# Kernel optimization log

Hardware: AMD Instinct MI355X
Metric: run time of the kernel (lower is better)

Reference implementation:

```python
import jax, jax.numpy as jnp
import numpy as np


def setup_inputs() -> dict:
    key = jax.random.key(0)
    ks = jax.random.split(key, 5)
    bt, c, h, w = 64, 64, 32, 32
    x = jax.random.normal(ks[0], (bt, c, h, w), dtype=jnp.float32)
    qkv_w = jax.random.normal(ks[1], (3 * c, c), dtype=jnp.float32) * 0.05
    qkv_b = jax.random.normal(ks[2], (3 * c,), dtype=jnp.float32) * 0.05
    tqk_w = jax.random.normal(ks[3], (2 * c, c, 3, 1, 1), dtype=jnp.float32) * 0.05
    tqk_b = jax.random.normal(ks[4], (2 * c,), dtype=jnp.float32) * 0.05
    return {"x": x, "qkv_w": qkv_w, "qkv_b": qkv_b,
            "tqk_w": tqk_w, "tqk_b": tqk_b, "n_segment": 8}


def reference(x, qkv_w, qkv_b, tqk_w, tqk_b, n_segment):
    bt, c, h, w = x.shape
    t = n_segment
    b = bt // t
    n = h * w
    scale = c ** (-0.5)

    # 1x1 conv -> qkv, then tokens: [bt, n, c]
    qkv = jnp.einsum('bchw,oc->bohw', x, qkv_w) + qkv_b[None, :, None, None]
    q, k, v = jnp.split(qkv, 3, axis=1)
    q, k, v = (a.transpose(0, 2, 3, 1).reshape(bt, n, c) for a in (q, k, v))

    # pixel (spatial) attention over n tokens
    pixel_dots = jnp.einsum('bic,bjc->bij', q, k) * scale          # [bt, n, n]
    pixel_attn = jax.nn.softmax(pixel_dots, axis=-1)
    pixel_out = jnp.einsum('bij,bjd->bid', pixel_attn, v)          # [bt, n, c]

    # channel attention over c channels
    chan_dots = jnp.einsum('bic,bik->bck', q, k) * scale           # [bt, c, c]
    chan_attn = jax.nn.softmax(chan_dots, axis=-1)
    chan_out = jnp.einsum('bij,bdj->bdi', chan_attn, v)            # [bt, n, c]

    x_hat = pixel_out + chan_out                                   # [bt, n, c]
    # '(b t) (h w) c -> b c t h w'
    x_hat = x_hat.reshape(b, t, h, w, c).transpose(0, 4, 1, 2, 3)

    # Conv3d kernel (3,1,1), padding (1,0,0): temporal-only conv
    t_qk = jax.lax.conv_general_dilated(
        x_hat, tqk_w, window_strides=(1, 1, 1),
        padding=[(1, 1), (0, 0), (0, 0)],
        dimension_numbers=('NCDHW', 'OIDHW', 'NCDHW'))
    t_qk = t_qk + tqk_b[None, :, None, None, None]                 # [b, 2c, t, h, w]
    tq, tk = jnp.split(t_qk, 2, axis=1)
    # 'b c t h w -> b t (c h w)'
    tq = tq.transpose(0, 2, 1, 3, 4).reshape(b, t, c * n)
    tk = tk.transpose(0, 2, 1, 3, 4).reshape(b, t, c * n)
    # tv: '(b t) (h w) c -> b t (c h w)'
    tv = v.reshape(b, t, h, w, c).transpose(0, 1, 4, 2, 3).reshape(b, t, c * n)

    dots = jnp.einsum('bid,bjd->bij', tq, tk)                      # [b, t, t] (no scale, as source)
    attn = jax.nn.softmax(dots, axis=-1)
    out = jnp.einsum('bkt,btd->bkd', attn, tv)                     # [b, t, c*n]
    out = out.reshape(b, t, c, h, w).reshape(bt, c, h, w)
    return out
```

## Files before the change

### kernel.cpp

```cpp
#include <hip/hip_runtime.h>

#define SCALE 0.125f

typedef _Float16 f16;
typedef _Float16 f16x8 __attribute__((ext_vector_type(8)));
typedef float f32x4 __attribute__((ext_vector_type(4)));

#define MFMA16(A,B,C) __builtin_amdgcn_mfma_f32_16x16x32_f16(A,B,C,0,0,0)

__device__ __forceinline__ float dp4(const float a[4], const float b[4], float acc) {
    acc = fmaf(a[0], b[0], acc);
    acc = fmaf(a[1], b[1], acc);
    acc = fmaf(a[2], b[2], acc);
    acc = fmaf(a[3], b[3], acc);
    return acc;
}

__device__ __forceinline__ int sw(int row) {
    return ((row & 7) ^ ((row >> 3) & 7)) << 4;
}

__global__ __launch_bounds__(256) void k_qkv(const float* __restrict__ x,
                                             const float* __restrict__ w,
                                             const float* __restrict__ bias,
                                             f16* __restrict__ q,
                                             f16* __restrict__ k,
                                             f16* __restrict__ v,
                                             f16* __restrict__ vt) {
    __shared__ float xs[64][64];
    __shared__ float ws[192][65];
    __shared__ f16 vts[4096];
    const int bt = blockIdx.y, pos0 = blockIdx.x * 64;
    const int tid = threadIdx.x;

    for (int it = 0; it < 16; ++it) {
        int idx = it * 256 + tid;
        int ci = idx >> 6, p = idx & 63;
        xs[ci][p] = x[(bt * 64 + ci) * 1024 + pos0 + p];
    }
    for (int it = 0; it < 48; ++it) {
        int idx = it * 256 + tid;
        ws[idx / 64][idx % 64] = w[idx];
    }
    __syncthreads();

    const int oc = tid & 63, grp = tid >> 6;
    float accq[16], acck[16], accv[16];
    const float bq = bias[oc], bk = bias[64 + oc], bv = bias[128 + oc];
#pragma unroll
    for (int p = 0; p < 16; ++p) { accq[p] = bq; acck[p] = bk; accv[p] = bv; }

    for (int ci = 0; ci < 64; ++ci) {
        float wq = ws[oc][ci], wk = ws[64 + oc][ci], wv = ws[128 + oc][ci];
        const float4* xr = (const float4*)&xs[ci][grp * 16];
#pragma unroll
        for (int p4 = 0; p4 < 4; ++p4) {
            float xa[4];
            *(float4*)xa = xr[p4];
#pragma unroll
            for (int e = 0; e < 4; ++e) {
                int p = p4 * 4 + e;
                accq[p] = fmaf(wq, xa[e], accq[p]);
                acck[p] = fmaf(wk, xa[e], acck[p]);
                accv[p] = fmaf(wv, xa[e], accv[p]);
            }
        }
    }
#pragma unroll
    for (int p = 0; p < 16; ++p) {
        int pos = pos0 + grp * 16 + p;
        int base = (bt * 1024 + pos) * 64 + oc;
        f16 vh = (f16)accv[p];
        q[base] = (f16)(accq[p] * SCALE);
        k[base] = (f16)acck[p];
        v[base] = vh;
        int col = grp * 16 + p;
        *(f16*)((char*)vts + oc * 128 + ((col * 2) ^ sw(oc))) = vh;
    }
    __syncthreads();
#pragma unroll
    for (int it = 0; it < 2; ++it) {
        int s = it * 256 + tid;
        int row = s >> 3, c8 = s & 7;
        f16x8 val = *(const f16x8*)((char*)vts + row * 128 + ((c8 * 16) ^ sw(row)));
        *(f16x8*)(vt + (bt * 64 + row) * 1024 + pos0 + c8 * 8) = val;
    }
}

__global__ __launch_bounds__(256) void k_chan_part(const f16* __restrict__ q,
                                                   const f16* __restrict__ k,
                                                   float* __restrict__ partials) {
    __shared__ float qs[64][68];
    __shared__ float ks[64][68];
    const int pc = blockIdx.x, bt = blockIdx.y, tid = threadIdx.x;
    const int ti = tid >> 4, tj = tid & 15;
    float acc[4][4] = {{0.f}};

    for (int ch = 0; ch < 4; ++ch) {
        int p0 = pc * 256 + ch * 64;
        __syncthreads();
        for (int it = 0; it < 2; ++it) {
            int e8 = it * 256 + tid;
            int p = e8 >> 3, c8 = e8 & 7;
            f16x8 qv = *(const f16x8*)(q + (bt * 1024 + p0 + p) * 64 + c8 * 8);
            f16x8 kv = *(const f16x8*)(k + (bt * 1024 + p0 + p) * 64 + c8 * 8);
            float4 qlo = make_float4((float)qv[0], (float)qv[1], (float)qv[2], (float)qv[3]);
            float4 qhi = make_float4((float)qv[4], (float)qv[5], (float)qv[6], (float)qv[7]);
            float4 klo = make_float4((float)kv[0], (float)kv[1], (float)kv[2], (float)kv[3]);
            float4 khi = make_float4((float)kv[4], (float)kv[5], (float)kv[6], (float)kv[7]);
            *(float4*)&qs[p][c8 * 8]     = qlo;
            *(float4*)&qs[p][c8 * 8 + 4] = qhi;
            *(float4*)&ks[p][c8 * 8]     = klo;
            *(float4*)&ks[p][c8 * 8 + 4] = khi;
        }
        __syncthreads();
#pragma unroll 8
        for (int p = 0; p < 64; ++p) {
            float qa[4], ka[4];
            *(float4*)qa = *(const float4*)&qs[p][ti * 4];
            *(float4*)ka = *(const float4*)&ks[p][tj * 4];
#pragma unroll
            for (int r = 0; r < 4; ++r)
#pragma unroll
                for (int c = 0; c < 4; ++c)
                    acc[r][c] = fmaf(qa[r], ka[c], acc[r][c]);
        }
    }
#pragma unroll
    for (int r = 0; r < 4; ++r) {
        float4 o4 = make_float4(acc[r][0], acc[r][1], acc[r][2], acc[r][3]);
        *(float4*)&partials[((bt * 4 + pc) * 64 + ti * 4 + r) * 64 + tj * 4] = o4;
    }
}

__global__ __launch_bounds__(256) void k_chan_red(const float* __restrict__ partials,
                                                  f16* __restrict__ cattn) {
    const int bt = blockIdx.x, tid = threadIdx.x;
    const int i = tid >> 2, q4 = tid & 3;
    float s[16];
#pragma unroll
    for (int jj = 0; jj < 16; ++jj) s[jj] = 0.f;
#pragma unroll
    for (int pc = 0; pc < 4; ++pc) {
        const float4* src = (const float4*)(partials + ((bt * 4 + pc) * 64 + i) * 64 + q4 * 16);
#pragma unroll
        for (int f4 = 0; f4 < 4; ++f4) {
            float a[4];
            *(float4*)a = src[f4];
#pragma unroll
            for (int e = 0; e < 4; ++e) s[f4 * 4 + e] += a[e];
        }
    }
    float m = -1e30f;
#pragma unroll
    for (int jj = 0; jj < 16; ++jj) m = fmaxf(m, s[jj]);
    m = fmaxf(m, __shfl_xor(m, 1, 64));
    m = fmaxf(m, __shfl_xor(m, 2, 64));
    float e[16], sum = 0.f;
#pragma unroll
    for (int jj = 0; jj < 16; ++jj) { e[jj] = __expf(s[jj] - m); sum += e[jj]; }
    sum += __shfl_xor(sum, 1, 64);
    sum += __shfl_xor(sum, 2, 64);
    float inv = 1.f / sum;
    f16x8 o0, o1;
#pragma unroll
    for (int jj = 0; jj < 8; ++jj) { o0[jj] = (f16)(e[jj] * inv); o1[jj] = (f16)(e[8 + jj] * inv); }
    f16* dst = cattn + (bt * 64 + i) * 64 + q4 * 16;
    *(f16x8*)dst = o0;
    *(f16x8*)(dst + 8) = o1;
}

__global__ __launch_bounds__(256) void k_pixel(const f16* __restrict__ q,
                                               const f16* __restrict__ k,
                                               const f16* __restrict__ v,
                                               const f16* __restrict__ vt,
                                               const f16* __restrict__ cattn,
                                               f16* __restrict__ xh,
                                               f16* __restrict__ xl) {
    __shared__ f16 kv_s[2][8192];
    __shared__ f16 p_s[8192];

    const int bt = blockIdx.x, row0 = blockIdx.y * 128;
    const int tid = threadIdx.x;
    const int wv = tid >> 6;
    const int ln = tid & 15;
    const int kgrp = (tid >> 4) & 3;
    const int r2 = tid >> 3, c8 = tid & 7;

    f16x8 k0, k1, v0, v1;
    const f16* kbase = k + bt * 1024 * 64;
    const f16* vtbase = vt + (size_t)bt * 65536;

    auto issue = [&](int ch) {
        const f16* kg = kbase + ch * 64 * 64;
        const f16* vtg = vtbase + ch * 64;
        k0 = *(const f16x8*)(kg + r2 * 64 + c8 * 8);
        k1 = *(const f16x8*)(kg + (r2 + 32) * 64 + c8 * 8);
        v0 = *(const f16x8*)(vtg + r2 * 1024 + c8 * 8);
        v1 = *(const f16x8*)(vtg + (r2 + 32) * 1024 + c8 * 8);
    };
    auto commit = [&](int buf) {
        char* kb = (char*)&kv_s[buf][0];
        char* vb = (char*)&kv_s[buf][4096];
        *(f16x8*)(kb + r2 * 128 + ((c8 * 16) ^ sw(r2))) = k0;
        *(f16x8*)(kb + (r2 + 32) * 128 + ((c8 * 16) ^ sw(r2 + 32))) = k1;
        *(f16x8*)(vb + r2 * 128 + ((c8 * 16) ^ sw(r2))) = v0;
        *(f16x8*)(vb + (r2 + 32) * 128 + ((c8 * 16) ^ sw(r2 + 32))) = v1;
    };

    issue(0);
    {
        const f16* qg = q + (bt * 1024 + row0) * 64;
#pragma unroll
        for (int p = 0; p < 4; ++p) {
            int e8 = p * 256 + tid;
            int rr = e8 >> 3, cc = e8 & 7;
            f16x8 val = *(const f16x8*)(qg + rr * 64 + cc * 8);
            *(f16x8*)((char*)p_s + rr * 128 + ((cc * 16) ^ sw(rr))) = val;
        }
    }
    __syncthreads();
    f16x8 qa[2][2];
#pragma unroll
    for (int rt = 0; rt < 2; ++rt) {
        int rr = rt * 64 + 16 * wv + ln;
#pragma unroll
        for (int kb = 0; kb < 2; ++kb)
            qa[rt][kb] = *(const f16x8*)((char*)p_s + rr * 128 + (((kb * 4 + kgrp) * 16) ^ sw(rr)));
    }
    commit(0);
    issue(1);
    __syncthreads();

    f32x4 out[2][4];
    float lr[2][4];
#pragma unroll
    for (int rt = 0; rt < 2; ++rt)
#pragma unroll
        for (int ct = 0; ct < 4; ++ct) {
            out[rt][ct] = (f32x4){0.f, 0.f, 0.f, 0.f};
            lr[rt][ct] = 0.f;
        }

    for (int ch = 0; ch < 16; ++ch) {
        const char* kb = (const char*)&kv_s[ch & 1][0];
        const char* vb = (const char*)&kv_s[ch & 1][4096];

        f16x8 kf[4][2];
#pragma unroll
        for (int jt = 0; jt < 4; ++jt)
#pragma unroll
            for (int kb2 = 0; kb2 < 2; ++kb2) {
                int jr = jt * 16 + ln;
                kf[jt][kb2] = *(const f16x8*)(kb + jr * 128 + (((kb2 * 4 + kgrp) * 16) ^ sw(jr)));
            }
#pragma unroll
        for (int rt = 0; rt < 2; ++rt) {
            f32x4 sx[4];
#pragma unroll
            for (int jt = 0; jt < 4; ++jt) sx[jt] = (f32x4){0.f, 0.f, 0.f, 0.f};
#pragma unroll
            for (int jt = 0; jt < 4; ++jt)
#pragma unroll
                for (int kb2 = 0; kb2 < 2; ++kb2)
                    sx[jt] = MFMA16(qa[rt][kb2], kf[jt][kb2], sx[jt]);
#pragma unroll
            for (int jt = 0; jt < 4; ++jt)
#pragma unroll
                for (int r = 0; r < 4; ++r) {
                    float p = __expf(sx[jt][r]);
                    lr[rt][r] += p;
                    int prow = rt * 64 + 16 * wv + kgrp * 4 + r;
                    int pcol = jt * 16 + ln;
                    *(f16*)((char*)p_s + prow * 128 + ((pcol * 2) ^ sw(prow))) = (f16)p;
                }
        }
        f16x8 vf[4][2];
#pragma unroll
        for (int ct = 0; ct < 4; ++ct)
#pragma unroll
            for (int kb2 = 0; kb2 < 2; ++kb2) {
                int cr = ct * 16 + ln;
                vf[ct][kb2] = *(const f16x8*)(vb + cr * 128 + (((kb2 * 4 + kgrp) * 16) ^ sw(cr)));
            }
#pragma unroll
        for (int rt = 0; rt < 2; ++rt) {
            int rr = rt * 64 + 16 * wv + ln;
            f16x8 pa[2];
#pragma unroll
            for (int kb2 = 0; kb2 < 2; ++kb2)
                pa[kb2] = *(const f16x8*)((char*)p_s + rr * 128 + (((kb2 * 4 + kgrp) * 16) ^ sw(rr)));
#pragma unroll
            for (int ct = 0; ct < 4; ++ct)
#pragma unroll
                for (int kb2 = 0; kb2 < 2; ++kb2)
                    out[rt][ct] = MFMA16(pa[kb2], vf[ct][kb2], out[rt][ct]);
        }
        if (ch < 15) {
            commit((ch + 1) & 1);
            if (ch < 14) issue(ch + 2);
        }
        __syncthreads();
    }

#pragma unroll
    for (int mask = 1; mask < 16; mask <<= 1)
#pragma unroll
        for (int rt = 0; rt < 2; ++rt)
#pragma unroll
            for (int r = 0; r < 4; ++r) lr[rt][r] += __shfl_xor(lr[rt][r], mask, 64);
#pragma unroll
    for (int rt = 0; rt < 2; ++rt)
#pragma unroll
        for (int r = 0; r < 4; ++r) {
            float inv = 1.f / lr[rt][r];
#pragma unroll
            for (int ct = 0; ct < 4; ++ct) out[rt][ct][r] *= inv;
        }

    {
        f16* cs = &kv_s[0][0];
        const f16* cg = cattn + bt * 4096;
#pragma unroll
        for (int p = 0; p < 2; ++p) {
            int e8 = p * 256 + tid;
            int rr = e8 >> 3, cc = e8 & 7;
            f16x8 cv = *(const f16x8*)(cg + rr * 64 + cc * 8);
            *(f16x8*)((char*)cs + rr * 128 + ((cc * 16) ^ sw(rr))) = cv;
        }
        const f16* vg = v + (bt * 1024 + row0) * 64;
#pragma unroll
        for (int p = 0; p < 4; ++p) {
            int e8 = p * 256 + tid;
            int rr = e8 >> 3, cc = e8 & 7;
            f16x8 vv = *(const f16x8*)(vg + rr * 64 + cc * 8);
            *(f16x8*)((char*)p_s + rr * 128 + ((cc * 16) ^ sw(rr))) = vv;
        }
    }
    __syncthreads();
    {
        const char* cs = (const char*)&kv_s[0][0];
        f16x8 cb[4][2];
#pragma unroll
        for (int it = 0; it < 4; ++it)
#pragma unroll
            for (int kb2 = 0; kb2 < 2; ++kb2) {
                int ir = it * 16 + ln;
                cb[it][kb2] = *(const f16x8*)(cs + ir * 128 + (((kb2 * 4 + kgrp) * 16) ^ sw(ir)));
            }
#pragma unroll
        for (int rt = 0; rt < 2; ++rt) {
            int rr = rt * 64 + 16 * wv + ln;
            f16x8 va[2];
#pragma unroll
            for (int kb2 = 0; kb2 < 2; ++kb2)
                va[kb2] = *(const f16x8*)((char*)p_s + rr * 128 + (((kb2 * 4 + kgrp) * 16) ^ sw(rr)));
#pragma unroll
            for (int it = 0; it < 4; ++it)
#pragma unroll
                for (int kb2 = 0; kb2 < 2; ++kb2)
                    out[rt][it] = MFMA16(va[kb2], cb[it][kb2], out[rt][it]);
        }
    }

#pragma unroll
    for (int rt = 0; rt < 2; ++rt)
#pragma unroll
        for (int ct = 0; ct < 4; ++ct)
#pragma unroll
            for (int r = 0; r < 4; ++r) {
                float val = out[rt][ct][r];
                f16 h = (f16)val;
                int idx = (bt * 1024 + row0 + rt * 64 + 16 * wv + kgrp * 4 + r) * 64 + ct * 16 + ln;
                xh[idx] = h;
                xl[idx] = (f16)(val - (float)h);
            }
}

__global__ void k_wprep(const float* __restrict__ w, f16* __restrict__ wsplit) {
    int d = blockIdx.x * 256 + threadIdx.x;
    int j = d & 7, oc = (d >> 3) & 127, kg = (d >> 10) & 3, kc = d >> 12;
    int K = kc * 32 + kg * 8 + j;
    int dt = K >> 6, ci = K & 63;
    float wf = w[(oc * 64 + ci) * 3 + dt];
    f16 h = (f16)wf;
    wsplit[d] = h;
    wsplit[24576 + d] = (f16)(wf - (float)h);
}

__global__ __launch_bounds__(256) void k_tconv(const f16* __restrict__ xh,
                                               const f16* __restrict__ xl,
                                               const f16* __restrict__ wsplit,
                                               const float* __restrict__ bias,
                                               float* __restrict__ tq,
                                               float* __restrict__ tk) {
    __shared__ f16 xs[2][3][4096];
    const int bt = blockIdx.y, pos0 = blockIdx.x * 64;
    const int b = bt >> 3, t = bt & 7;
    const int tid = threadIdx.x;
    const int wvid = tid >> 6, ln = tid & 15, kgrp = (tid >> 4) & 3;

    for (int dt = 0; dt < 3; ++dt) {
        int tt = t + dt - 1;
        bool ok = (tt >= 0) && (tt < 8);
        const f16* srch = xh + ((b * 8 + tt) * 1024 + pos0) * 64;
        const f16* srcl = xl + ((b * 8 + tt) * 1024 + pos0) * 64;
#pragma unroll
        for (int p = 0; p < 2; ++p) {
            int e8 = p * 256 + tid;
            int r2 = e8 >> 3, c8 = e8 & 7;
            f16x8 vh = {0, 0, 0, 0, 0, 0, 0, 0};
            f16x8 vl = {0, 0, 0, 0, 0, 0, 0, 0};
            if (ok) {
                vh = *(const f16x8*)(srch + r2 * 64 + c8 * 8);
                vl = *(const f16x8*)(srcl + r2 * 64 + c8 * 8);
            }
            int byte = r2 * 128 + ((c8 * 16) ^ sw(r2));
            *(f16x8*)((char*)&xs[0][dt][0] + byte) = vh;
            *(f16x8*)((char*)&xs[1][dt][0] + byte) = vl;
        }
    }

    f16x8 bh[2][6], bl[2][6];
#pragma unroll
    for (int og = 0; og < 2; ++og) {
        int oc = wvid * 32 + og * 16 + ln;
#pragma unroll
        for (int kc = 0; kc < 6; ++kc) {
            int idx = (kc * 4 + kgrp) * 1024 + oc * 8;
            bh[og][kc] = *(const f16x8*)(wsplit + idx);
            bl[og][kc] = *(const f16x8*)(wsplit + 24576 + idx);
        }
    }
    __syncthreads();

#pragma unroll
    for (int pg = 0; pg < 4; ++pg) {
        f16x8 ah[6], al[6];
        int rr = pg * 16 + ln;
#pragma unroll
        for (int kc = 0; kc < 6; ++kc) {
            int dt = kc >> 1;
            int ci0 = (kc & 1) * 32 + kgrp * 8;
            int byte = rr * 128 + ((ci0 * 2) ^ sw(rr));
            ah[kc] = *(const f16x8*)((char*)&xs[0][dt][0] + byte);
            al[kc] = *(const f16x8*)((char*)&xs[1][dt][0] + byte);
        }
#pragma unroll
        for (int og = 0; og < 2; ++og) {
            int oc = wvid * 32 + og * 16 + ln;
            float bv = bias[oc];
            f32x4 acc = {bv, bv, bv, bv};
#pragma unroll
            for (int kc = 0; kc < 6; ++kc) {
                acc = MFMA16(ah[kc], bh[og][kc], acc);
                acc = MFMA16(al[kc], bh[og][kc], acc);
                acc = MFMA16(ah[kc], bl[og][kc], acc);
            }
            float* dst = (oc < 64) ? tq : tk;
            int orow = oc & 63;
            int pos = pos0 + pg * 16 + kgrp * 4;
            *(float4*)&dst[(bt * 64 + orow) * 1024 + pos] =
                make_float4(acc[0], acc[1], acc[2], acc[3]);
        }
    }
}

__global__ __launch_bounds__(256) void k_tdots(const float* __restrict__ tq,
                                               const float* __restrict__ tk,
                                               float* __restrict__ partials) {
    __shared__ float qs[8][516];
    __shared__ float ks[8][516];
    const int ch = blockIdx.x, b = blockIdx.y;
    const int tid = threadIdx.x;
    const int d0 = ch * 512;

    for (int it = 0; it < 4; ++it) {
        int f4 = it * 256 + tid;
        int i = f4 >> 7, d4 = f4 & 127;
        *(float4*)&qs[i][d4 * 4] = *(const float4*)(tq + (size_t)(b * 8 + i) * 65536 + d0 + d4 * 4);
        *(float4*)&ks[i][d4 * 4] = *(const float4*)(tk + (size_t)(b * 8 + i) * 65536 + d0 + d4 * 4);
    }
    __syncthreads();

    const int p = tid >> 2, sub = tid & 3;
    const int i = p >> 3, j = p & 7;
    float acc = 0.f;
#pragma unroll 8
    for (int d4 = 0; d4 < 32; ++d4) {
        int off = (d4 * 4 + sub) * 4;
        float qa[4], ka[4];
        *(float4*)qa = *(const float4*)&qs[i][off];
        *(float4*)ka = *(const float4*)&ks[j][off];
        acc = dp4(qa, ka, acc);
    }
    acc += __shfl_xor(acc, 1, 64);
    acc += __shfl_xor(acc, 2, 64);
    if (sub == 0) partials[(b * 128 + ch) * 64 + p] = acc;
}

__global__ void k_tsm(const float* __restrict__ partials, float* __restrict__ ta) {
    const int b = blockIdx.x, tid = threadIdx.x;
    float s = 0.f;
    for (int ch = 0; ch < 128; ++ch) s += partials[(b * 128 + ch) * 64 + tid];
    float m = s;
#pragma unroll
    for (int mask = 1; mask < 8; mask <<= 1) m = fmaxf(m, __shfl_xor(m, mask, 64));
    float e = __expf(s - m);
    float sum = e;
#pragma unroll
    for (int mask = 1; mask < 8; mask <<= 1) sum += __shfl_xor(sum, mask, 64);
    ta[b * 64 + tid] = e / sum;
}

__global__ __launch_bounds__(256) void k_tout(const f16* __restrict__ v,
                                              const float* __restrict__ ta,
                                              float* __restrict__ outp) {
    __shared__ float ot[64][65];
    const int pt = blockIdx.x, kk = blockIdx.y, b = blockIdx.z;
    const int pos0 = pt * 64;
    const int tid = threadIdx.x;
    const int cc = tid & 63, grp = tid >> 6;
    float a[8];
#pragma unroll
    for (int t = 0; t < 8; ++t) a[t] = ta[(b * 8 + kk) * 8 + t];
    float acc[16] = {0.f};
#pragma unroll
    for (int t = 0; t < 8; ++t) {
        const f16* vb = v + ((size_t)(b * 8 + t) * 1024 + pos0) * 64 + cc;
#pragma unroll
        for (int pp = 0; pp < 16; ++pp)
            acc[pp] = fmaf(a[t], (float)vb[(grp * 16 + pp) * 64], acc[pp]);
    }
#pragma unroll
    for (int pp = 0; pp < 16; ++pp) ot[cc][grp * 16 + pp] = acc[pp];
    __syncthreads();
    for (int it = 0; it < 16; ++it) {
        int idx = it * 256 + tid;
        int c2 = idx >> 6, p2 = idx & 63;
        outp[((b * 8 + kk) * 64 + c2) * 1024 + pos0 + p2] = ot[c2][p2];
    }
}

extern "C" void kernel_launch(void* const* d_in, const int* in_sizes, int n_in,
                              void* d_out, int out_size, void* d_ws, size_t ws_size,
                              hipStream_t stream) {
    const float* x     = (const float*)d_in[0];
    const float* qkv_w = (const float*)d_in[1];
    const float* qkv_b = (const float*)d_in[2];
    const float* tqk_w = (const float*)d_in[3];
    const float* tqk_b = (const float*)d_in[4];
    float* outp = (float*)d_out;

    char* wsb = (char*)d_ws;
    f16*   q        = (f16*)wsb;
    f16*   k        = (f16*)(wsb + (8u << 20));
    f16*   v        = (f16*)(wsb + (16u << 20));
    f16*   cattn    = (f16*)(wsb + (24u << 20));
    float* tpart    = (float*)(wsb + (24u << 20) + (1u << 19));
    float* ta       = (float*)(wsb + (24u << 20) + (1u << 19) + (1u << 18));
    f16*   wsplit   = (f16*)(wsb + (24u << 20) + (1u << 19) + (1u << 18) + 8192);
    f16*   xhat_hi  = (f16*)(wsb + (25u << 20));
    f16*   xhat_lo  = (f16*)(wsb + (33u << 20));
    float* cpart    = (float*)(wsb + (41u << 20));
    float* tq       = (float*)wsb;
    float* tk       = (float*)(wsb + (41u << 20));
    f16*   vt       = (f16*)(wsb + (57u << 20));

    k_qkv      <<<dim3(16, 64), 256, 0, stream>>>(x, qkv_w, qkv_b, q, k, v, vt);
    k_wprep    <<<dim3(96), 256, 0, stream>>>(tqk_w, wsplit);
    k_chan_part<<<dim3(4, 64), 256, 0, stream>>>(q, k, cpart);
    k_chan_red <<<dim3(64), 256, 0, stream>>>(cpart, cattn);
    k_pixel    <<<dim3(64, 8), 256, 0, stream>>>(q, k, v, vt, cattn, xhat_hi, xhat_lo);
    k_tconv    <<<dim3(16, 64), 256, 0, stream>>>(xhat_hi, xhat_lo, wsplit, tqk_b, tq, tk);
    k_tdots    <<<dim3(128, 8), 256, 0, stream>>>(tq, tk, tpart);
    k_tsm      <<<dim3(8), 64, 0, stream>>>(tpart, ta);
    k_tout     <<<dim3(16, 8, 8), 256, 0, stream>>>(v, ta, outp);
}
```

Before: 183.7 us.

## Fuse weight prep into qkv, softmax into tout, transpose pixel S layout

Folds the temporal-conv weight split into extra blocks of the qkv kernel and folds the temporal softmax reduction into the output kernel, removing two launches. The output kernel now handles four query frames per block, reusing each V load across them. The pixel attention kernel computes S transposed (K as the A operand), so each lane holds contiguous P columns. It writes them as packed f16x2 into a padded 144-byte-stride buffer and reduces row sums with fewer shuffles. The cost is redundant partial-sum reduction per tout block and more registers in tout.

```diff
diff --git a/kernel.cpp b/kernel.cpp
--- a/kernel.cpp
+++ b/kernel.cpp
@@ -3,6 +3,7 @@
 #define SCALE 0.125f
 
 typedef _Float16 f16;
+typedef _Float16 f16x2 __attribute__((ext_vector_type(2)));
 typedef _Float16 f16x8 __attribute__((ext_vector_type(8)));
 typedef float f32x4 __attribute__((ext_vector_type(4)));
 
@@ -23,15 +24,31 @@
 __global__ __launch_bounds__(256) void k_qkv(const float* __restrict__ x,
                                              const float* __restrict__ w,
                                              const float* __restrict__ bias,
+                                             const float* __restrict__ tqkw,
                                              f16* __restrict__ q,
                                              f16* __restrict__ k,
                                              f16* __restrict__ v,
-                                             f16* __restrict__ vt) {
+                                             f16* __restrict__ vt,
+                                             f16* __restrict__ wsplit) {
+    const int tid = threadIdx.x;
+    if (blockIdx.y == 64) {
+#pragma unroll
+        for (int it = 0; it < 6; ++it) {
+            int d = blockIdx.x * 1536 + it * 256 + tid;
+            int j = d & 7, oc = (d >> 3) & 127, kg = (d >> 10) & 3, kc = d >> 12;
+            int K = kc * 32 + kg * 8 + j;
+            int dt = K >> 6, ci = K & 63;
+            float wf = tqkw[(oc * 64 + ci) * 3 + dt];
+            f16 h = (f16)wf;
+            wsplit[d] = h;
+            wsplit[24576 + d] = (f16)(wf - (float)h);
+        }
+        return;
+    }
     __shared__ float xs[64][64];
     __shared__ float ws[192][65];
     __shared__ f16 vts[4096];
     const int bt = blockIdx.y, pos0 = blockIdx.x * 64;
-    const int tid = threadIdx.x;
 
     for (int it = 0; it < 16; ++it) {
         int idx = it * 256 + tid;
@@ -178,7 +195,7 @@
                                                f16* __restrict__ xh,
                                                f16* __restrict__ xl) {
     __shared__ f16 kv_s[2][8192];
-    __shared__ f16 p_s[8192];
+    __shared__ char p_raw[18432];
 
     const int bt = blockIdx.x, row0 = blockIdx.y * 128;
     const int tid = threadIdx.x;
@@ -216,7 +233,7 @@
             int e8 = p * 256 + tid;
             int rr = e8 >> 3, cc = e8 & 7;
             f16x8 val = *(const f16x8*)(qg + rr * 64 + cc * 8);
-            *(f16x8*)((char*)p_s + rr * 128 + ((cc * 16) ^ sw(rr))) = val;
+            *(f16x8*)(p_raw + rr * 128 + ((cc * 16) ^ sw(rr))) = val;
         }
     }
     __syncthreads();
@@ -226,21 +243,18 @@
         int rr = rt * 64 + 16 * wv + ln;
 #pragma unroll
         for (int kb = 0; kb < 2; ++kb)
-            qa[rt][kb] = *(const f16x8*)((char*)p_s + rr * 128 + (((kb * 4 + kgrp) * 16) ^ sw(rr)));
+            qa[rt][kb] = *(const f16x8*)(p_raw + rr * 128 + (((kb * 4 + kgrp) * 16) ^ sw(rr)));
     }
     commit(0);
     issue(1);
     __syncthreads();
 
     f32x4 out[2][4];
-    float lr[2][4];
+    float lr[2] = {0.f, 0.f};
 #pragma unroll
     for (int rt = 0; rt < 2; ++rt)
 #pragma unroll
-        for (int ct = 0; ct < 4; ++ct) {
-            out[rt][ct] = (f32x4){0.f, 0.f, 0.f, 0.f};
-            lr[rt][ct] = 0.f;
-        }
+        for (int ct = 0; ct < 4; ++ct) out[rt][ct] = (f32x4){0.f, 0.f, 0.f, 0.f};
 
     for (int ch = 0; ch < 16; ++ch) {
         const char* kb = (const char*)&kv_s[ch & 1][0];
@@ -256,6 +270,8 @@
             }
 #pragma unroll
         for (int rt = 0; rt < 2; ++rt) {
+            int prow = rt * 64 + wv * 16 + ln;
+            char* pb = p_raw + prow * 144;
             f32x4 sx[4];
 #pragma unroll
             for (int jt = 0; jt < 4; ++jt) sx[jt] = (f32x4){0.f, 0.f, 0.f, 0.f};
@@ -263,17 +279,18 @@
             for (int jt = 0; jt < 4; ++jt)
 #pragma unroll
                 for (int kb2 = 0; kb2 < 2; ++kb2)
-                    sx[jt] = MFMA16(qa[rt][kb2], kf[jt][kb2], sx[jt]);
-#pragma unroll
-            for (int jt = 0; jt < 4; ++jt)
-#pragma unroll
-                for (int r = 0; r < 4; ++r) {
-                    float p = __expf(sx[jt][r]);
-                    lr[rt][r] += p;
-                    int prow = rt * 64 + 16 * wv + kgrp * 4 + r;
-                    int pcol = jt * 16 + ln;
-                    *(f16*)((char*)p_s + prow * 128 + ((pcol * 2) ^ sw(prow))) = (f16)p;
-                }
+                    sx[jt] = MFMA16(kf[jt][kb2], qa[rt][kb2], sx[jt]);
+#pragma unroll
+            for (int jt = 0; jt < 4; ++jt) {
+                float p0 = __expf(sx[jt][0]), p1 = __expf(sx[jt][1]);
+                float p2 = __expf(sx[jt][2]), p3 = __expf(sx[jt][3]);
+                lr[rt] += (p0 + p1) + (p2 + p3);
+                f16x2 w0, w1;
+                w0[0] = (f16)p0; w0[1] = (f16)p1;
+                w1[0] = (f16)p2; w1[1] = (f16)p3;
+                *(f16x2*)(pb + (jt * 8 + kgrp * 2) * 4) = w0;
+                *(f16x2*)(pb + (jt * 8 + kgrp * 2 + 1) * 4) = w1;
+            }
         }
         f16x8 vf[4][2];
 #pragma unroll
@@ -285,11 +302,11 @@
             }
 #pragma unroll
         for (int rt = 0; rt < 2; ++rt) {
-            int rr = rt * 64 + 16 * wv + ln;
+            int prow = rt * 64 + wv * 16 + ln;
             f16x8 pa[2];
 #pragma unroll
             for (int kb2 = 0; kb2 < 2; ++kb2)
-                pa[kb2] = *(const f16x8*)((char*)p_s + rr * 128 + (((kb2 * 4 + kgrp) * 16) ^ sw(rr)));
+                pa[kb2] = *(const f16x8*)(p_raw + prow * 144 + (kb2 * 16 + kgrp * 4) * 4);
 #pragma unroll
             for (int ct = 0; ct < 4; ++ct)
 #pragma unroll
@@ -303,20 +320,21 @@
         __syncthreads();
     }
 
-#pragma unroll
-    for (int mask = 1; mask < 16; mask <<= 1)
-#pragma unroll
-        for (int rt = 0; rt < 2; ++rt)
-#pragma unroll
-            for (int r = 0; r < 4; ++r) lr[rt][r] += __shfl_xor(lr[rt][r], mask, 64);
-#pragma unroll
-    for (int rt = 0; rt < 2; ++rt)
-#pragma unroll
-        for (int r = 0; r < 4; ++r) {
-            float inv = 1.f / lr[rt][r];
-#pragma unroll
-            for (int ct = 0; ct < 4; ++ct) out[rt][ct][r] *= inv;
-        }
+    float invr[2][4];
+#pragma unroll
+    for (int rt = 0; rt < 2; ++rt) {
+        float l = lr[rt];
+        l += __shfl_xor(l, 16, 64);
+        l += __shfl_xor(l, 32, 64);
+        float inv = 1.f / l;
+#pragma unroll
+        for (int r = 0; r < 4; ++r)
+            invr[rt][r] = __shfl(inv, kgrp * 4 + r, 64);
+#pragma unroll
+        for (int r = 0; r < 4; ++r)
+#pragma unroll
+            for (int ct = 0; ct < 4; ++ct) out[rt][ct][r] *= invr[rt][r];
+    }
 
     {
         f16* cs = &kv_s[0][0];
@@ -334,7 +352,7 @@
             int e8 = p * 256 + tid;
             int rr = e8 >> 3, cc = e8 & 7;
             f16x8 vv = *(const f16x8*)(vg + rr * 64 + cc * 8);
-            *(f16x8*)((char*)p_s + rr * 128 + ((cc * 16) ^ sw(rr))) = vv;
+            *(f16x8*)(p_raw + rr * 128 + ((cc * 16) ^ sw(rr))) = vv;
         }
     }
     __syncthreads();
@@ -354,7 +372,7 @@
             f16x8 va[2];
 #pragma unroll
             for (int kb2 = 0; kb2 < 2; ++kb2)
-                va[kb2] = *(const f16x8*)((char*)p_s + rr * 128 + (((kb2 * 4 + kgrp) * 16) ^ sw(rr)));
+                va[kb2] = *(const f16x8*)(p_raw + rr * 128 + (((kb2 * 4 + kgrp) * 16) ^ sw(rr)));
 #pragma unroll
             for (int it = 0; it < 4; ++it)
 #pragma unroll
@@ -375,17 +393,6 @@
                 xh[idx] = h;
                 xl[idx] = (f16)(val - (float)h);
             }
-}
-
-__global__ void k_wprep(const float* __restrict__ w, f16* __restrict__ wsplit) {
-    int d = blockIdx.x * 256 + threadIdx.x;
-    int j = d & 7, oc = (d >> 3) & 127, kg = (d >> 10) & 3, kc = d >> 12;
-    int K = kc * 32 + kg * 8 + j;
-    int dt = K >> 6, ci = K & 63;
-    float wf = w[(oc * 64 + ci) * 3 + dt];
-    f16 h = (f16)wf;
-    wsplit[d] = h;
-    wsplit[24576 + d] = (f16)(wf - (float)h);
 }
 
 __global__ __launch_bounds__(256) void k_tconv(const f16* __restrict__ xh,
@@ -499,46 +506,77 @@
     if (sub == 0) partials[(b * 128 + ch) * 64 + p] = acc;
 }
 
-__global__ void k_tsm(const float* __restrict__ partials, float* __restrict__ ta) {
-    const int b = blockIdx.x, tid = threadIdx.x;
-    float s = 0.f;
-    for (int ch = 0; ch < 128; ++ch) s += partials[(b * 128 + ch) * 64 + tid];
-    float m = s;
-#pragma unroll
-    for (int mask = 1; mask < 8; mask <<= 1) m = fmaxf(m, __shfl_xor(m, mask, 64));
-    float e = __expf(s - m);
-    float sum = e;
-#pragma unroll
-    for (int mask = 1; mask < 8; mask <<= 1) sum += __shfl_xor(sum, mask, 64);
-    ta[b * 64 + tid] = e / sum;
-}
-
 __global__ __launch_bounds__(256) void k_tout(const f16* __restrict__ v,
-                                              const float* __restrict__ ta,
+                                              const float* __restrict__ partials,
                                               float* __restrict__ outp) {
+    __shared__ float sred[32][9];
+    __shared__ float ta_s[4][8];
     __shared__ float ot[64][65];
-    const int pt = blockIdx.x, kk = blockIdx.y, b = blockIdx.z;
+    const int pt = blockIdx.x, kq = blockIdx.y, b = blockIdx.z;
     const int pos0 = pt * 64;
     const int tid = threadIdx.x;
+
+    {
+        const int pair = tid & 31, grp8 = tid >> 5;
+        const int i = kq * 4 + (pair >> 3), j = pair & 7;
+        float s = 0.f;
+#pragma unroll
+        for (int c = 0; c < 16; ++c)
+            s += partials[(b * 128 + grp8 * 16 + c) * 64 + i * 8 + j];
+        sred[pair][grp8] = s;
+    }
+    __syncthreads();
+    if (tid < 32) {
+        float t = 0.f;
+#pragma unroll
+        for (int g = 0; g < 8; ++g) t += sred[tid][g];
+        float m = t;
+        m = fmaxf(m, __shfl_xor(m, 1, 64));
+        m = fmaxf(m, __shfl_xor(m, 2, 64));
+        m = fmaxf(m, __shfl_xor(m, 4, 64));
+        float e = __expf(t - m);
+        float se = e;
+        se += __shfl_xor(se, 1, 64);
+        se += __shfl_xor(se, 2, 64);
+        se += __shfl_xor(se, 4, 64);
+        ta_s[tid >> 3][tid & 7] = e / se;
+    }
+    __syncthreads();
+
     const int cc = tid & 63, grp = tid >> 6;
-    float a[8];
-#pragma unroll
-    for (int t = 0; t < 8; ++t) a[t] = ta[(b * 8 + kk) * 8 + t];
-    float acc[16] = {0.f};
+    float tar[4][8];
+#pragma unroll
+    for (int kk = 0; kk < 4; ++kk)
+#pragma unroll
+        for (int t = 0; t < 8; ++t) tar[kk][t] = ta_s[kk][t];
+    float acc[4][16];
+#pragma unroll
+    for (int kk = 0; kk < 4; ++kk)
+#pragma unroll
+        for (int pp = 0; pp < 16; ++pp) acc[kk][pp] = 0.f;
 #pragma unroll
     for (int t = 0; t < 8; ++t) {
         const f16* vb = v + ((size_t)(b * 8 + t) * 1024 + pos0) * 64 + cc;
 #pragma unroll
-        for (int pp = 0; pp < 16; ++pp)
-            acc[pp] = fmaf(a[t], (float)vb[(grp * 16 + pp) * 64], acc[pp]);
-    }
-#pragma unroll
-    for (int pp = 0; pp < 16; ++pp) ot[cc][grp * 16 + pp] = acc[pp];
-    __syncthreads();
-    for (int it = 0; it < 16; ++it) {
-        int idx = it * 256 + tid;
-        int c2 = idx >> 6, p2 = idx & 63;
-        outp[((b * 8 + kk) * 64 + c2) * 1024 + pos0 + p2] = ot[c2][p2];
+        for (int pp = 0; pp < 16; ++pp) {
+            float vv = (float)vb[(grp * 16 + pp) * 64];
+#pragma unroll
+            for (int kk = 0; kk < 4; ++kk)
+                acc[kk][pp] = fmaf(tar[kk][t], vv, acc[kk][pp]);
+        }
+    }
+#pragma unroll
+    for (int kk = 0; kk < 4; ++kk) {
+        __syncthreads();
+#pragma unroll
+        for (int pp = 0; pp < 16; ++pp) ot[cc][grp * 16 + pp] = acc[kk][pp];
+        __syncthreads();
+        float* dst = outp + ((size_t)(b * 8 + kq * 4 + kk) * 64) * 1024 + pos0;
+        for (int it = 0; it < 16; ++it) {
+            int idx = it * 256 + tid;
+            int c2 = idx >> 6, p2 = idx & 63;
+            dst[c2 * 1024 + p2] = ot[c2][p2];
+        }
     }
 }
 
@@ -558,7 +596,6 @@
     f16*   v        = (f16*)(wsb + (16u << 20));
     f16*   cattn    = (f16*)(wsb + (24u << 20));
     float* tpart    = (float*)(wsb + (24u << 20) + (1u << 19));
-    float* ta       = (float*)(wsb + (24u << 20) + (1u << 19) + (1u << 18));
     f16*   wsplit   = (f16*)(wsb + (24u << 20) + (1u << 19) + (1u << 18) + 8192);
     f16*   xhat_hi  = (f16*)(wsb + (25u << 20));
     f16*   xhat_lo  = (f16*)(wsb + (33u << 20));
@@ -567,13 +604,11 @@
     float* tk       = (float*)(wsb + (41u << 20));
     f16*   vt       = (f16*)(wsb + (57u << 20));
 
-    k_qkv      <<<dim3(16, 64), 256, 0, stream>>>(x, qkv_w, qkv_b, q, k, v, vt);
-    k_wprep    <<<dim3(96), 256, 0, stream>>>(tqk_w, wsplit);
+    k_qkv      <<<dim3(16, 65), 256, 0, stream>>>(x, qkv_w, qkv_b, tqk_w, q, k, v, vt, wsplit);
     k_chan_part<<<dim3(4, 64), 256, 0, stream>>>(q, k, cpart);
     k_chan_red <<<dim3(64), 256, 0, stream>>>(cpart, cattn);
     k_pixel    <<<dim3(64, 8), 256, 0, stream>>>(q, k, v, vt, cattn, xhat_hi, xhat_lo);
     k_tconv    <<<dim3(16, 64), 256, 0, stream>>>(xhat_hi, xhat_lo, wsplit, tqk_b, tq, tk);
     k_tdots    <<<dim3(128, 8), 256, 0, stream>>>(tq, tk, tpart);
-    k_tsm      <<<dim3(8), 64, 0, stream>>>(tpart, ta);
-    k_tout     <<<dim3(16, 8, 8), 256, 0, stream>>>(v, ta, outp);
-}
+    k_tout     <<<dim3(16, 2, 8), 256, 0, stream>>>(v, tpart, outp);
+}
```

Result: faster. 178.3 us (-2.9%).
